# Performance work log

Measured on AMD Instinct MI355X. Metric: run time of the kernel, lower is better.

## Reference

```python
import math
import jax, jax.numpy as jnp
import numpy as np

VMIN, VMAX, NUM_BINS = 0.0, 1.0, 64
BIN_WIDTH = (VMAX - VMIN) / NUM_BINS
SIGMA = BIN_WIDTH * (1.0 / (2.0 * math.sqrt(2.0 * math.log(2.0))))
EPS = 1e-10


def setup_inputs() -> dict:
    key = jax.random.key(0)
    kx, ky = jax.random.split(key)
    shape = (2, 1, 96, 96, 96)
    x = jax.random.uniform(kx, shape, dtype=jnp.float32)
    y = jax.random.uniform(ky, shape, dtype=jnp.float32)
    return {"x": x, "y": y}


def _gauss_win(v, bins):
    # v: (N, P), bins: (B,) -> (N, B, P)
    d = v[:, None, :] - bins[None, :, None]
    # NOTE: faithful to source: exp(.)/sqrt(2*pi) * sigma (multiplies by sigma)
    return jnp.exp(-(d * d) / (2.0 * SIGMA * SIGMA)) / math.sqrt(2.0 * math.pi) * SIGMA


def reference(x, y):
    N = x.shape[0]
    xf = x.reshape(N, -1)  # (N, P); dim=1 channel folded into P
    yf = y.reshape(N, -1)
    bins = jnp.linspace(VMIN, VMAX, NUM_BINS, dtype=x.dtype)
    win_x = _gauss_win(xf, bins)  # (N, B, P)
    win_y = _gauss_win(yf, bins)  # (N, B, P)
    hist_joint = jnp.einsum('nbp,ncp->nbc', win_x, win_y)  # (N, B, B)
    hist_norm = hist_joint.sum(axis=(1, 2)) + EPS
    p_joint = hist_joint / hist_norm[:, None, None]
    p_x = p_joint.sum(axis=2)
    p_y = p_joint.sum(axis=1)
    ent_x = -jnp.sum(p_x * jnp.log(p_x + EPS), axis=1)
    ent_y = -jnp.sum(p_y * jnp.log(p_y + EPS), axis=1)
    ent_joint = -jnp.sum(p_joint * jnp.log(p_joint + EPS), axis=(1, 2))
    # normalised=True branch
    return -jnp.mean((ent_x + ent_y) / ent_joint)
```

## Files before the change

kernel.cpp:

```cpp
#include <hip/hip_runtime.h>
#include <math.h>


#define NBINS 64
#define BK 240
#define LDA (BK + 8)
#define NKB (BK / 16)

typedef _Float16 half8   __attribute__((ext_vector_type(8)));
typedef float    floatx16 __attribute__((ext_vector_type(16)));

static constexpr double kSigmaD = 0.015625 / 2.3548200450309493;
static constexpr double kAcD    = (1.0 / (63.0 * 63.0)) / (2.0 * kSigmaD * kSigmaD);
static constexpr float  kAc     = (float)kAcD;
static constexpr float  kEps    = 1e-10f;

__global__ void zero_ws_kernel(float* __restrict__ hist, float* __restrict__ out, int n) {
    int i = blockIdx.x * blockDim.x + threadIdx.x;
    if (i < n) hist[i] = 0.0f;
    if (i == 0) out[0] = 0.0f;
}

__global__ __launch_bounds__(256) void hist_gemm_kernel(
        const float* __restrict__ x, const float* __restrict__ y,
        float* __restrict__ hist, int P, int elemsPerBlock) {
    __shared__ _Float16 Ax[NBINS * LDA];
    __shared__ _Float16 By[NBINS * LDA];

    const int t    = threadIdx.x;
    const int lane = t & 63;
    const int wave = t >> 6;
    const int qi   = wave >> 1;
    const int qj   = wave & 1;
    const int n    = blockIdx.y;

    {
        float* a4 = (float*)Ax;
        float* b4 = (float*)By;
        const int ndw = NBINS * LDA / 2;
        for (int i = t; i < ndw; i += 256) { a4[i] = 0.0f; b4[i] = 0.0f; }
    }

    floatx16 acc = {};
    const float* __restrict__ xp = x + (size_t)n * P;
    const float* __restrict__ yp = y + (size_t)n * P;
    const int base    = blockIdx.x * elemsPerBlock;
    const int nElems  = elemsPerBlock;
    const int nChunks = (nElems + BK - 1) / BK;

    int pcx = 2, pcy = 2;
    __syncthreads();

    for (int c = 0; c < nChunks; ++c) {
        const int off = c * BK + t;
        float wx[5], wy[5];
        int cx = 2, cy = 2;
        const bool valid = (t < BK) && (off < nElems);
        if (valid) {
            const float vx = xp[base + off] * 63.0f;
            const float vy = yp[base + off] * 63.0f;
            cx = min(max((int)(vx + 0.5f), 2), 61);
            cy = min(max((int)(vy + 0.5f), 2), 61);
            const float dx = vx - (float)cx;
            const float dy = vy - (float)cy;
#pragma unroll
            for (int k = 0; k < 5; ++k) {
                const float ddx = dx - (float)(k - 2);
                const float ddy = dy - (float)(k - 2);
                wx[k] = __expf(-kAc * ddx * ddx);
                wy[k] = __expf(-kAc * ddy * ddy);
            }
        } else {
#pragma unroll
            for (int k = 0; k < 5; ++k) { wx[k] = 0.0f; wy[k] = 0.0f; }
        }

        if (t < BK) {
#pragma unroll
            for (int k = 0; k < 5; ++k) {
                Ax[(pcx - 2 + k) * LDA + t] = (_Float16)0.0f;
                By[(pcy - 2 + k) * LDA + t] = (_Float16)0.0f;
            }
#pragma unroll
            for (int k = 0; k < 5; ++k) {
                Ax[(cx - 2 + k) * LDA + t] = (_Float16)wx[k];
                By[(cy - 2 + k) * LDA + t] = (_Float16)wy[k];
            }
        }
        pcx = cx; pcy = cy;
        __syncthreads();

        const int rA = qi * 32 + (lane & 31);
        const int rB = qj * 32 + (lane & 31);
        const int kq = 8 * (lane >> 5);
#pragma unroll
        for (int kb = 0; kb < NKB; ++kb) {
            const half8 a = *(const half8*)&Ax[rA * LDA + kb * 16 + kq];
            const half8 b = *(const half8*)&By[rB * LDA + kb * 16 + kq];
            acc = __builtin_amdgcn_mfma_f32_32x32x16_f16(a, b, acc, 0, 0, 0);
        }
        __syncthreads();
    }

    float* __restrict__ gh = hist + (size_t)n * NBINS * NBINS;
#pragma unroll
    for (int r = 0; r < 16; ++r) {
        const int row = qi * 32 + (r & 3) + 8 * (r >> 2) + 4 * (lane >> 5);
        const int col = qj * 32 + (lane & 31);
        atomicAdd(&gh[row * NBINS + col], acc[r]);
    }
}

__device__ __forceinline__ float block_sum_bcast(float v, float* sm) {
#pragma unroll
    for (int off = 32; off > 0; off >>= 1) v += __shfl_down(v, off, 64);
    __syncthreads();
    const int lane = threadIdx.x & 63;
    const int wid  = threadIdx.x >> 6;
    if (lane == 0) sm[wid] = v;
    __syncthreads();
    return sm[0] + sm[1] + sm[2] + sm[3];
}

__global__ __launch_bounds__(256) void finalize_kernel(
        const float* __restrict__ hist, float* __restrict__ out) {
    __shared__ float sm[4];
    __shared__ float sx[NBINS];
    __shared__ float sy[NBINS];

    const int n = blockIdx.x;
    const float* __restrict__ h = hist + (size_t)n * NBINS * NBINS;

    float s = 0.0f;
    for (int i = threadIdx.x; i < NBINS * NBINS; i += 256) s += h[i];
    const float S = block_sum_bcast(s, sm) + kEps;
    const float invS = 1.0f / S;

    float ej = 0.0f;
    for (int i = threadIdx.x; i < NBINS * NBINS; i += 256) {
        const float p = h[i] * invS;
        ej += p * __logf(p + kEps);
    }

    if (threadIdx.x < NBINS) {
        float px = 0.0f;
        const float* rp = &h[threadIdx.x * NBINS];
        for (int c = 0; c < NBINS; c++) px += rp[c];
        px *= invS;
        sx[threadIdx.x] = px * __logf(px + kEps);
    } else if (threadIdx.x < 2 * NBINS) {
        const int c = threadIdx.x - NBINS;
        float py = 0.0f;
        for (int b = 0; b < NBINS; b++) py += h[b * NBINS + c];
        py *= invS;
        sy[c] = py * __logf(py + kEps);
    }

    const float EJ = block_sum_bcast(ej, sm);
    const float mx = (threadIdx.x < NBINS) ? sx[threadIdx.x] : 0.0f;
    const float my = (threadIdx.x < NBINS) ? sy[threadIdx.x] : 0.0f;
    const float EX = block_sum_bcast(mx, sm);
    const float EY = block_sum_bcast(my, sm);

    if (threadIdx.x == 0) atomicAdd(out, -0.5f * ((EX + EY) / EJ));
}

extern "C" void kernel_launch(void* const* d_in, const int* in_sizes, int n_in,
                              void* d_out, int out_size, void* d_ws, size_t ws_size,
                              hipStream_t stream) {
    const float* x = (const float*)d_in[0];
    const float* y = (const float*)d_in[1];
    float* hist = (float*)d_ws;
    float* out  = (float*)d_out;

    const int N = 2;
    const int P = in_sizes[0] / N;
    const int blocksPerN = 256;
    const int elemsPerBlock = P / blocksPerN;

    const int histElems = N * NBINS * NBINS;
    zero_ws_kernel<<<(histElems + 255) / 256, 256, 0, stream>>>(hist, out, histElems);

    dim3 grid(blocksPerN, N);
    hist_gemm_kernel<<<grid, 256, 0, stream>>>(x, y, hist, P, elemsPerBlock);

    finalize_kernel<<<2, 256, 0, stream>>>(hist, out);
}
```

Before: 103.0 us.

## Give each wave its own LDS tiles to drop block barriers, prefetch next chunk

Restructures the histogram GEMM so each wave owns private 64-row A/B tiles in LDS. Each wave processes 64-element chunks and computes the full 64x64 output with four MFMA accumulators, which removes the per-chunk __syncthreads. The next chunk's inputs are loaded one iteration ahead in software. At the end the two waves' partials are reduced in LDS, so a block issues one set of global atomics instead of four waves each doing their own. The grid doubles to 512 blocks of 128 threads. The cost is more accumulator registers per wave and a smaller K per MFMA batch.

```diff
diff --git a/kernel.cpp b/kernel.cpp
--- a/kernel.cpp
+++ b/kernel.cpp
@@ -3,11 +3,10 @@
 
 
 #define NBINS 64
-#define BK 240
-#define LDA (BK + 8)
-#define NKB (BK / 16)
-
-typedef _Float16 half8   __attribute__((ext_vector_type(8)));
+#define LDA2 72
+#define TILEH (NBINS * LDA2)
+
+typedef _Float16 half8    __attribute__((ext_vector_type(8)));
 typedef float    floatx16 __attribute__((ext_vector_type(16)));
 
 static constexpr double kSigmaD = 0.015625 / 2.3548200450309493;
@@ -21,48 +20,59 @@
     if (i == 0) out[0] = 0.0f;
 }
 
-__global__ __launch_bounds__(256) void hist_gemm_kernel(
+__global__ __launch_bounds__(128, 2) void hist_gemm_kernel(
         const float* __restrict__ x, const float* __restrict__ y,
-        float* __restrict__ hist, int P, int elemsPerBlock) {
-    __shared__ _Float16 Ax[NBINS * LDA];
-    __shared__ _Float16 By[NBINS * LDA];
+        float* __restrict__ hist, int P, int elemsPerWave) {
+    __shared__ __align__(16) _Float16 tiles[2][2][NBINS][LDA2];
 
     const int t    = threadIdx.x;
     const int lane = t & 63;
     const int wave = t >> 6;
-    const int qi   = wave >> 1;
-    const int qj   = wave & 1;
     const int n    = blockIdx.y;
 
+    _Float16* __restrict__ Ax = &tiles[wave][0][0][0];
+    _Float16* __restrict__ By = &tiles[wave][1][0][0];
+
     {
-        float* a4 = (float*)Ax;
-        float* b4 = (float*)By;
-        const int ndw = NBINS * LDA / 2;
-        for (int i = t; i < ndw; i += 256) { a4[i] = 0.0f; b4[i] = 0.0f; }
-    }
-
-    floatx16 acc = {};
+        float4* p4 = (float4*)Ax;
+        const int n16 = 2 * TILEH * 2 / 16;
+        for (int i = lane; i < n16; i += 64) p4[i] = float4{0.f, 0.f, 0.f, 0.f};
+    }
+
+    floatx16 acc[2][2] = {};
     const float* __restrict__ xp = x + (size_t)n * P;
     const float* __restrict__ yp = y + (size_t)n * P;
-    const int base    = blockIdx.x * elemsPerBlock;
-    const int nElems  = elemsPerBlock;
-    const int nChunks = (nElems + BK - 1) / BK;
+
+    const int waveBase = (blockIdx.x * 2 + wave) * elemsPerWave;
+    int lim = P - waveBase;
+    if (lim > elemsPerWave) lim = elemsPerWave;
+    const int nChunks = (elemsPerWave + 63) / 64;
+
+#define GLOAD(c2, ox, oy) do {                                   \
+        int off_ = (c2) * 64 + lane;                             \
+        int g_ = waveBase + ((off_ < lim) ? off_ : 0);           \
+        g_ = min(g_, P - 1);                                     \
+        ox = xp[g_]; oy = yp[g_];                                \
+    } while (0)
 
     int pcx = 2, pcy = 2;
-    __syncthreads();
+    float vx, vy;
+    GLOAD(0, vx, vy);
 
     for (int c = 0; c < nChunks; ++c) {
-        const int off = c * BK + t;
+        float nvx = 0.f, nvy = 0.f;
+        if (c + 1 < nChunks) GLOAD(c + 1, nvx, nvy);
+
+        const bool valid = (c * 64 + lane) < lim;
         float wx[5], wy[5];
         int cx = 2, cy = 2;
-        const bool valid = (t < BK) && (off < nElems);
         if (valid) {
-            const float vx = xp[base + off] * 63.0f;
-            const float vy = yp[base + off] * 63.0f;
-            cx = min(max((int)(vx + 0.5f), 2), 61);
-            cy = min(max((int)(vy + 0.5f), 2), 61);
-            const float dx = vx - (float)cx;
-            const float dy = vy - (float)cy;
+            const float sx = vx * 63.0f;
+            const float sy = vy * 63.0f;
+            cx = min(max((int)(sx + 0.5f), 2), 61);
+            cy = min(max((int)(sy + 0.5f), 2), 61);
+            const float dx = sx - (float)cx;
+            const float dy = sy - (float)cy;
 #pragma unroll
             for (int k = 0; k < 5; ++k) {
                 const float ddx = dx - (float)(k - 2);
@@ -75,39 +85,56 @@
             for (int k = 0; k < 5; ++k) { wx[k] = 0.0f; wy[k] = 0.0f; }
         }
 
-        if (t < BK) {
-#pragma unroll
-            for (int k = 0; k < 5; ++k) {
-                Ax[(pcx - 2 + k) * LDA + t] = (_Float16)0.0f;
-                By[(pcy - 2 + k) * LDA + t] = (_Float16)0.0f;
+#pragma unroll
+        for (int k = 0; k < 5; ++k) {
+            Ax[(pcx - 2 + k) * LDA2 + lane] = (_Float16)0.0f;
+            By[(pcy - 2 + k) * LDA2 + lane] = (_Float16)0.0f;
+        }
+#pragma unroll
+        for (int k = 0; k < 5; ++k) {
+            Ax[(cx - 2 + k) * LDA2 + lane] = (_Float16)wx[k];
+            By[(cy - 2 + k) * LDA2 + lane] = (_Float16)wy[k];
+        }
+        pcx = cx; pcy = cy;
+
+        const int mrow = lane & 31;
+        const int kq   = 8 * (lane >> 5);
+        const _Float16* pa = &Ax[mrow * LDA2 + kq];
+        const _Float16* pb = &By[mrow * LDA2 + kq];
+#pragma unroll
+        for (int kb = 0; kb < 4; ++kb) {
+            const half8 a0 = *(const half8*)(pa + kb * 16);
+            const half8 a1 = *(const half8*)(pa + 32 * LDA2 + kb * 16);
+            const half8 b0 = *(const half8*)(pb + kb * 16);
+            const half8 b1 = *(const half8*)(pb + 32 * LDA2 + kb * 16);
+            acc[0][0] = __builtin_amdgcn_mfma_f32_32x32x16_f16(a0, b0, acc[0][0], 0, 0, 0);
+            acc[0][1] = __builtin_amdgcn_mfma_f32_32x32x16_f16(a0, b1, acc[0][1], 0, 0, 0);
+            acc[1][0] = __builtin_amdgcn_mfma_f32_32x32x16_f16(a1, b0, acc[1][0], 0, 0, 0);
+            acc[1][1] = __builtin_amdgcn_mfma_f32_32x32x16_f16(a1, b1, acc[1][1], 0, 0, 0);
+        }
+
+        vx = nvx; vy = nvy;
+    }
+#undef GLOAD
+
+    float* wsum = (float*)&tiles[wave][0][0][0];
+#pragma unroll
+    for (int qi = 0; qi < 2; ++qi)
+#pragma unroll
+        for (int qj = 0; qj < 2; ++qj)
+#pragma unroll
+            for (int r = 0; r < 16; ++r) {
+                const int row = qi * 32 + (r & 3) + 8 * (r >> 2) + 4 * (lane >> 5);
+                const int col = qj * 32 + (lane & 31);
+                wsum[row * NBINS + col] = acc[qi][qj][r];
             }
-#pragma unroll
-            for (int k = 0; k < 5; ++k) {
-                Ax[(cx - 2 + k) * LDA + t] = (_Float16)wx[k];
-                By[(cy - 2 + k) * LDA + t] = (_Float16)wy[k];
-            }
-        }
-        pcx = cx; pcy = cy;
-        __syncthreads();
-
-        const int rA = qi * 32 + (lane & 31);
-        const int rB = qj * 32 + (lane & 31);
-        const int kq = 8 * (lane >> 5);
-#pragma unroll
-        for (int kb = 0; kb < NKB; ++kb) {
-            const half8 a = *(const half8*)&Ax[rA * LDA + kb * 16 + kq];
-            const half8 b = *(const half8*)&By[rB * LDA + kb * 16 + kq];
-            acc = __builtin_amdgcn_mfma_f32_32x32x16_f16(a, b, acc, 0, 0, 0);
-        }
-        __syncthreads();
-    }
+    __syncthreads();
 
     float* __restrict__ gh = hist + (size_t)n * NBINS * NBINS;
-#pragma unroll
-    for (int r = 0; r < 16; ++r) {
-        const int row = qi * 32 + (r & 3) + 8 * (r >> 2) + 4 * (lane >> 5);
-        const int col = qj * 32 + (lane & 31);
-        atomicAdd(&gh[row * NBINS + col], acc[r]);
+    const float* w0 = (const float*)&tiles[0][0][0][0];
+    const float* w1 = (const float*)&tiles[1][0][0][0];
+    for (int i = t; i < NBINS * NBINS; i += 128) {
+        atomicAdd(&gh[i], w0[i] + w1[i]);
     }
 }
 
@@ -175,14 +202,14 @@
 
     const int N = 2;
     const int P = in_sizes[0] / N;
-    const int blocksPerN = 256;
-    const int elemsPerBlock = P / blocksPerN;
+    const int blocksPerN   = 512;
+    const int elemsPerWave = P / (blocksPerN * 2);
 
     const int histElems = N * NBINS * NBINS;
     zero_ws_kernel<<<(histElems + 255) / 256, 256, 0, stream>>>(hist, out, histElems);
 
     dim3 grid(blocksPerN, N);
-    hist_gemm_kernel<<<grid, 256, 0, stream>>>(x, y, hist, P, elemsPerBlock);
+    hist_gemm_kernel<<<grid, 128, 0, stream>>>(x, y, hist, P, elemsPerWave);
 
     finalize_kernel<<<2, 256, 0, stream>>>(hist, out);
 }
```

Result: no change. 103.6 us (+0.6%).
